# Kernel optimization log

Measured on AMD Instinct MI355X. Metric: run time of the kernel, lower is better.

## Reference

```python
import jax, jax.numpy as jnp
import numpy as np

WIN = (9, 9, 9)
EPS = 1e-05


def setup_inputs() -> dict:
    key = jax.random.key(0)
    k1, k2 = jax.random.split(key)
    shape = (2, 1, 160, 160, 160)  # [B, C=1, D, H, W]
    x = jax.random.normal(k1, shape, dtype=jnp.float32)
    y = jax.random.normal(k2, shape, dtype=jnp.float32)
    return {"x": x, "y": y}


def _convn(z, kernel):
    # dense 3D box-sum conv, VALID (inputs are pre-padded), NCDHW layout
    return jax.lax.conv_general_dilated(
        z, kernel, window_strides=(1, 1, 1), padding='VALID',
        dimension_numbers=('NCDHW', 'OIDHW', 'NCDHW'))


def reference(x, y):
    p = tuple(w // 2 for w in WIN)  # (4, 4, 4)
    pad_cfg = ((0, 0), (0, 0), (p[0], p[0]), (p[1], p[1]), (p[2], p[2]))
    kernel = jnp.ones((1, 1) + WIN, dtype=x.dtype)

    x_pad = jnp.pad(x, pad_cfg, mode='edge')      # replicate padding
    y_pad = jnp.pad(y, pad_cfg, mode='edge')
    ones_pad = jnp.pad(jnp.ones_like(x), pad_cfg, mode='edge')

    N = _convn(ones_pad, kernel)                  # local window counts (all = 729 here)
    xm = _convn(x_pad, kernel) / N                # local mean of x
    ym = _convn(y_pad, kernel) / N                # local mean of y
    x2 = _convn(x_pad * x_pad, kernel) / N        # local E[x^2]
    y2 = _convn(y_pad * y_pad, kernel) / N        # local E[y^2]
    xy = _convn(x_pad * y_pad, kernel) / N        # local E[xy]

    cross = xy - xm * ym
    var_x = x2 - xm * xm
    var_y = y2 - ym * ym
    ncc = cross * cross / (var_x * var_y + EPS)
    return -jnp.mean(ncc)
```

## Files before the change

kernel.cpp:

```cpp
#include <hip/hip_runtime.h>

#define DIM 160
#define SLICE (DIM * DIM)
#define TH 16
#define TW 16
#define CD 20
#define NS (CD + 8)

#define HP 492
#define HR 20
#define HIDX(c,i,j) ((c)*HP + (i)*HR + (j))
#define UIDX(c,i,j) ((c)*260 + (i)*16 + (j))

#define WSLIDE(dst, V0,V1,V2,V3,V4,V5,V6,V7,V8,V9,V10,V11) do {            \
    float s_ = (V0)+(V1)+(V2)+(V3)+(V4)+(V5)+(V6)+(V7)+(V8);               \
    float4 o_; o_.x = s_;                                                  \
    s_ += (V9)  - (V0); o_.y = s_;                                         \
    s_ += (V10) - (V1); o_.z = s_;                                         \
    s_ += (V11) - (V2); o_.w = s_;                                         \
    (dst) = o_; } while (0)

static __device__ __forceinline__ void barrier_novm()
{
    asm volatile("s_waitcnt lgkmcnt(0)" ::: "memory");
    __builtin_amdgcn_s_barrier();
    asm volatile("" ::: "memory");
}

__global__ __launch_bounds__(256, 2)
void lncc_kernel(const float* __restrict__ x, const float* __restrict__ y,
                 float* __restrict__ out)
{
    __shared__ __align__(16) float H[2][5 * HP];
    __shared__ __align__(16) float U[2][5 * 260];
    __shared__ float wsum[4];

    const int t  = threadIdx.x;
    const int w0 = blockIdx.x * TW;
    const int h0 = blockIdx.y * TH;
    const int bz = blockIdx.z;
    const int b   = bz >> 3;
    const int zo0 = (bz & 7) * CD;

    const float* xb = x + (size_t)b * (DIM * SLICE);
    const float* yb = y + (size_t)b * (DIM * SLICE);

    const int lt  = t - 160;
    const int lrw = lt >> 2;
    const int lq  = lt & 3;
    const int ghr = min(max(h0 - 4 + lrw, 0), DIM - 1);
    const int rowoff = ghr * DIM;
    const int gws = w0 + 4 * lq - 4;
    const bool ok0 = (gws >= 0);
    const bool ok2 = (gws + 8 <= DIM - 4);
    const int jj = 4 * lq;

    const int hcc = t >> 3;
    const int hq  = (t >> 1) & 3;
    const int hh  = t & 1;
    const int hr0 = hh * 8;
    const int hjj = 4 * hq;

    const int i4 = t >> 4;
    const int j4 = t & 15;

    float hist[9][5];
    float rs[5] = {0.f, 0.f, 0.f, 0.f, 0.f};
    float acc = 0.f;

    float4 lX0, lX1, lX2, lY0, lY1, lY2;

    auto issue_loads = [&](int zsl) {
        const float* xs = xb + (size_t)zsl * SLICE + rowoff;
        const float* ys = yb + (size_t)zsl * SLICE + rowoff;
        lX1 = *reinterpret_cast<const float4*>(xs + gws + 4);
        lY1 = *reinterpret_cast<const float4*>(ys + gws + 4);
        if (ok0) {
            lX0 = *reinterpret_cast<const float4*>(xs + gws);
            lY0 = *reinterpret_cast<const float4*>(ys + gws);
        } else {
            const float v = xs[0];       lX0 = make_float4(v, v, v, v);
            const float w = ys[0];       lY0 = make_float4(w, w, w, w);
        }
        if (ok2) {
            lX2 = *reinterpret_cast<const float4*>(xs + gws + 8);
            lY2 = *reinterpret_cast<const float4*>(ys + gws + 8);
        } else {
            const float v = xs[DIM - 1]; lX2 = make_float4(v, v, v, v);
            const float w = ys[DIM - 1]; lY2 = make_float4(w, w, w, w);
        }
    };

    auto wsums_to = [&](float* Hb) {
        float4 o;
        WSLIDE(o, lX0.x,lX0.y,lX0.z,lX0.w, lX1.x,lX1.y,lX1.z,lX1.w,
                  lX2.x,lX2.y,lX2.z,lX2.w);
        *reinterpret_cast<float4*>(&Hb[HIDX(0, lrw, jj)]) = o;
        WSLIDE(o, lY0.x,lY0.y,lY0.z,lY0.w, lY1.x,lY1.y,lY1.z,lY1.w,
                  lY2.x,lY2.y,lY2.z,lY2.w);
        *reinterpret_cast<float4*>(&Hb[HIDX(1, lrw, jj)]) = o;
        float4 a0 = lX0 * lX0, a1 = lX1 * lX1, a2 = lX2 * lX2;
        WSLIDE(o, a0.x,a0.y,a0.z,a0.w, a1.x,a1.y,a1.z,a1.w, a2.x,a2.y,a2.z,a2.w);
        *reinterpret_cast<float4*>(&Hb[HIDX(2, lrw, jj)]) = o;
        a0 = lY0 * lY0; a1 = lY1 * lY1; a2 = lY2 * lY2;
        WSLIDE(o, a0.x,a0.y,a0.z,a0.w, a1.x,a1.y,a1.z,a1.w, a2.x,a2.y,a2.z,a2.w);
        *reinterpret_cast<float4*>(&Hb[HIDX(3, lrw, jj)]) = o;
        a0 = lX0 * lY0; a1 = lX1 * lY1; a2 = lX2 * lY2;
        WSLIDE(o, a0.x,a0.y,a0.z,a0.w, a1.x,a1.y,a1.z,a1.w, a2.x,a2.y,a2.z,a2.w);
        *reinterpret_cast<float4*>(&Hb[HIDX(4, lrw, jj)]) = o;
    };

    const int zfirst = zo0 - 4;
    auto zclamp = [&](int sl) { return min(max(zfirst + sl, 0), DIM - 1); };
    if (t >= 160) issue_loads(zclamp(0));

    for (int base = 0; base < 36; base += 18) {
        #pragma unroll
        for (int p = 0; p < 18; ++p) {
            const int i = base + p;
            if (i <= NS + 1) {
                if (i >= 2) {
                    const float* Ub = U[p & 1];
                    const int cp = (p + 7) % 9;
                    float u[5];
                    #pragma unroll
                    for (int c = 0; c < 5; ++c) {
                        u[c] = Ub[UIDX(c, i4, j4)];
                        rs[c] += u[c];
                        hist[cp][c] = u[c];
                    }
                    if (i >= 10) {
                        const float inv = 1.0f / 729.0f;
                        const float xm = rs[0] * inv, ym = rs[1] * inv;
                        const float x2 = rs[2] * inv, y2 = rs[3] * inv;
                        const float xy = rs[4] * inv;
                        const float cross = xy - xm * ym;
                        const float vx = x2 - xm * xm;
                        const float vy = y2 - ym * ym;
                        acc += cross * cross / (vx * vy + 1e-5f);
                        const int po = (cp + 1) % 9;
                        #pragma unroll
                        for (int c = 0; c < 5; ++c)
                            rs[c] -= hist[po][c];
                    }
                }
                if (i <= NS - 1 && t >= 160) {
                    wsums_to(H[p & 1]);
                    if (i <= NS - 2) issue_loads(zclamp(i + 1));
                }
                if (i >= 1 && i <= NS && t < 40) {
                    const float* Hb = H[(p + 1) & 1];
                    float* Ue = U[(p + 1) & 1];
                    float4 sum = make_float4(0.f, 0.f, 0.f, 0.f);
                    #pragma unroll
                    for (int k = 0; k < 9; ++k)
                        sum += *reinterpret_cast<const float4*>(&Hb[HIDX(hcc, hr0 + k, hjj)]);
                    *reinterpret_cast<float4*>(&Ue[UIDX(hcc, hr0, hjj)]) = sum;
                    #pragma unroll
                    for (int m = 1; m < 8; ++m) {
                        sum += *reinterpret_cast<const float4*>(&Hb[HIDX(hcc, hr0 + m + 8, hjj)])
                             - *reinterpret_cast<const float4*>(&Hb[HIDX(hcc, hr0 + m - 1, hjj)]);
                        *reinterpret_cast<float4*>(&Ue[UIDX(hcc, hr0 + m, hjj)]) = sum;
                    }
                }
                barrier_novm();
            }
        }
    }

    __syncthreads();
    #pragma unroll
    for (int off = 32; off > 0; off >>= 1)
        acc += __shfl_down(acc, off, 64);
    const int wave = t >> 6;
    if ((t & 63) == 0) wsum[wave] = acc;
    __syncthreads();
    if (t == 0) {
        const float s = wsum[0] + wsum[1] + wsum[2] + wsum[3];
        atomicAdd(out, -s * (1.0f / 8192000.0f));
    }
}

extern "C" void kernel_launch(void* const* d_in, const int* in_sizes, int n_in,
                              void* d_out, int out_size, void* d_ws, size_t ws_size,
                              hipStream_t stream)
{
    const float* x = (const float*)d_in[0];
    const float* y = (const float*)d_in[1];
    float* out = (float*)d_out;

    hipMemsetAsync(out, 0, sizeof(float), stream);

    dim3 grid(DIM / TW, DIM / TH, 2 * (DIM / CD));
    lncc_kernel<<<grid, 256, 0, stream>>>(x, y, out);
}
```

Baseline: 182.3 us.

## Double z-depth per block and prefetch two slices ahead with paired registers

```diff
diff --git a/kernel.cpp b/kernel.cpp
--- a/kernel.cpp
+++ b/kernel.cpp
@@ -4,7 +4,7 @@
 #define SLICE (DIM * DIM)
 #define TH 16
 #define TW 16
-#define CD 20
+#define CD 40
 #define NS (CD + 8)
 
 #define HP 492
@@ -39,8 +39,8 @@
     const int w0 = blockIdx.x * TW;
     const int h0 = blockIdx.y * TH;
     const int bz = blockIdx.z;
-    const int b   = bz >> 3;
-    const int zo0 = (bz & 7) * CD;
+    const int b   = bz >> 2;
+    const int zo0 = (bz & 3) * CD;
 
     const float* xb = x + (size_t)b * (DIM * SLICE);
     const float* yb = y + (size_t)b * (DIM * SLICE);
@@ -68,53 +68,58 @@
     float rs[5] = {0.f, 0.f, 0.f, 0.f, 0.f};
     float acc = 0.f;
 
-    float4 lX0, lX1, lX2, lY0, lY1, lY2;
-
-    auto issue_loads = [&](int zsl) {
+    float4 eX0, eX1, eX2, eY0, eY1, eY2;
+    float4 oX0, oX1, oX2, oY0, oY1, oY2;
+
+    auto issue_into = [&](int zsl, float4& X0, float4& X1, float4& X2,
+                                   float4& Y0, float4& Y1, float4& Y2) {
         const float* xs = xb + (size_t)zsl * SLICE + rowoff;
         const float* ys = yb + (size_t)zsl * SLICE + rowoff;
-        lX1 = *reinterpret_cast<const float4*>(xs + gws + 4);
-        lY1 = *reinterpret_cast<const float4*>(ys + gws + 4);
+        X1 = *reinterpret_cast<const float4*>(xs + gws + 4);
+        Y1 = *reinterpret_cast<const float4*>(ys + gws + 4);
         if (ok0) {
-            lX0 = *reinterpret_cast<const float4*>(xs + gws);
-            lY0 = *reinterpret_cast<const float4*>(ys + gws);
+            X0 = *reinterpret_cast<const float4*>(xs + gws);
+            Y0 = *reinterpret_cast<const float4*>(ys + gws);
         } else {
-            const float v = xs[0];       lX0 = make_float4(v, v, v, v);
-            const float w = ys[0];       lY0 = make_float4(w, w, w, w);
+            const float v = xs[0];       X0 = make_float4(v, v, v, v);
+            const float w = ys[0];       Y0 = make_float4(w, w, w, w);
         }
         if (ok2) {
-            lX2 = *reinterpret_cast<const float4*>(xs + gws + 8);
-            lY2 = *reinterpret_cast<const float4*>(ys + gws + 8);
+            X2 = *reinterpret_cast<const float4*>(xs + gws + 8);
+            Y2 = *reinterpret_cast<const float4*>(ys + gws + 8);
         } else {
-            const float v = xs[DIM - 1]; lX2 = make_float4(v, v, v, v);
-            const float w = ys[DIM - 1]; lY2 = make_float4(w, w, w, w);
+            const float v = xs[DIM - 1]; X2 = make_float4(v, v, v, v);
+            const float w = ys[DIM - 1]; Y2 = make_float4(w, w, w, w);
         }
     };
 
-    auto wsums_to = [&](float* Hb) {
+    auto wsums_to = [&](float* Hb,
+                        const float4& X0, const float4& X1, const float4& X2,
+                        const float4& Y0, const float4& Y1, const float4& Y2) {
         float4 o;
-        WSLIDE(o, lX0.x,lX0.y,lX0.z,lX0.w, lX1.x,lX1.y,lX1.z,lX1.w,
-                  lX2.x,lX2.y,lX2.z,lX2.w);
+        WSLIDE(o, X0.x,X0.y,X0.z,X0.w, X1.x,X1.y,X1.z,X1.w, X2.x,X2.y,X2.z,X2.w);
         *reinterpret_cast<float4*>(&Hb[HIDX(0, lrw, jj)]) = o;
-        WSLIDE(o, lY0.x,lY0.y,lY0.z,lY0.w, lY1.x,lY1.y,lY1.z,lY1.w,
-                  lY2.x,lY2.y,lY2.z,lY2.w);
+        WSLIDE(o, Y0.x,Y0.y,Y0.z,Y0.w, Y1.x,Y1.y,Y1.z,Y1.w, Y2.x,Y2.y,Y2.z,Y2.w);
         *reinterpret_cast<float4*>(&Hb[HIDX(1, lrw, jj)]) = o;
-        float4 a0 = lX0 * lX0, a1 = lX1 * lX1, a2 = lX2 * lX2;
+        float4 a0 = X0 * X0, a1 = X1 * X1, a2 = X2 * X2;
         WSLIDE(o, a0.x,a0.y,a0.z,a0.w, a1.x,a1.y,a1.z,a1.w, a2.x,a2.y,a2.z,a2.w);
         *reinterpret_cast<float4*>(&Hb[HIDX(2, lrw, jj)]) = o;
-        a0 = lY0 * lY0; a1 = lY1 * lY1; a2 = lY2 * lY2;
+        a0 = Y0 * Y0; a1 = Y1 * Y1; a2 = Y2 * Y2;
         WSLIDE(o, a0.x,a0.y,a0.z,a0.w, a1.x,a1.y,a1.z,a1.w, a2.x,a2.y,a2.z,a2.w);
         *reinterpret_cast<float4*>(&Hb[HIDX(3, lrw, jj)]) = o;
-        a0 = lX0 * lY0; a1 = lX1 * lY1; a2 = lX2 * lY2;
+        a0 = X0 * Y0; a1 = X1 * Y1; a2 = X2 * Y2;
         WSLIDE(o, a0.x,a0.y,a0.z,a0.w, a1.x,a1.y,a1.z,a1.w, a2.x,a2.y,a2.z,a2.w);
         *reinterpret_cast<float4*>(&Hb[HIDX(4, lrw, jj)]) = o;
     };
 
     const int zfirst = zo0 - 4;
     auto zclamp = [&](int sl) { return min(max(zfirst + sl, 0), DIM - 1); };
-    if (t >= 160) issue_loads(zclamp(0));
-
-    for (int base = 0; base < 36; base += 18) {
+    if (t >= 160) {
+        issue_into(zclamp(0), eX0, eX1, eX2, eY0, eY1, eY2);
+        issue_into(zclamp(1), oX0, oX1, oX2, oY0, oY1, oY2);
+    }
+
+    for (int base = 0; base < 54; base += 18) {
         #pragma unroll
         for (int p = 0; p < 18; ++p) {
             const int i = base + p;
@@ -145,8 +150,15 @@
                     }
                 }
                 if (i <= NS - 1 && t >= 160) {
-                    wsums_to(H[p & 1]);
-                    if (i <= NS - 2) issue_loads(zclamp(i + 1));
+                    if ((p & 1) == 0) {
+                        wsums_to(H[0], eX0, eX1, eX2, eY0, eY1, eY2);
+                        if (i <= NS - 3)
+                            issue_into(zclamp(i + 2), eX0, eX1, eX2, eY0, eY1, eY2);
+                    } else {
+                        wsums_to(H[1], oX0, oX1, oX2, oY0, oY1, oY2);
+                        if (i <= NS - 3)
+                            issue_into(zclamp(i + 2), oX0, oX1, oX2, oY0, oY1, oY2);
+                    }
                 }
                 if (i >= 1 && i <= NS && t < 40) {
                     const float* Hb = H[(p + 1) & 1];
```

Measured after the change: 171.0 us. 1.07x faster.
